# Optimization experiments

Measured on AMD Instinct MI355X. Metric: run time of the kernel, lower is better.

## Reference

```python
import jax, jax.numpy as jnp
import numpy as np
import math

NUM_HEADS = 20
HEAD_SIZE = 20  # newssize = 400
NEG_INF = -1e9


def setup_inputs() -> dict:
    key = jax.random.key(0)
    ks = jax.random.split(key, 10)
    B, S, L, V, D, M = 512, 100, 30, 50000, 400, 128
    user_click = jax.random.randint(ks[0], (B, S, L), 0, V)
    seq_len = jax.random.randint(ks[1], (B,), 1, S + 1)  # at least 1 valid click
    sc = 1.0 / math.sqrt(D)
    return {
        "user_click": user_click,
        "seq_len": seq_len,
        "emb_table": jax.random.normal(ks[2], (V, D), jnp.float32) * 0.02,
        "wq": jax.random.normal(ks[3], (D, D), jnp.float32) * sc,
        "wk": jax.random.normal(ks[4], (D, D), jnp.float32) * sc,
        "wv": jax.random.normal(ks[5], (D, D), jnp.float32) * sc,
        "fc1_w": jax.random.normal(ks[6], (D, M), jnp.float32) * sc,
        "fc1_b": jnp.zeros((M,), jnp.float32),
        "fc2_w": jax.random.normal(ks[7], (M, 1), jnp.float32) * (1.0 / math.sqrt(M)),
        "fc2_b": jnp.zeros((1,), jnp.float32),
    }


def reference(user_click, seq_len, emb_table, wq, wk, wv, fc1_w, fc1_b, fc2_w, fc2_b):
    B, S, L = user_click.shape
    D = emb_table.shape[1]
    H, Dh = NUM_HEADS, HEAD_SIZE

    # news encoder: mean-pooled token embeddings -> [B, S, D]
    click = jnp.take(emb_table, user_click.reshape(-1, L), axis=0).mean(axis=1)
    click = click.reshape(B, S, D)

    # mask: valid positions get +1.0 (as in the torch code), invalid -1e9
    valid = jnp.arange(S)[None, :] < seq_len[:, None]  # [B, S]
    mask = jnp.where(valid, 1.0, NEG_INF).astype(click.dtype)

    # multi-head self-attention over history
    q = (click @ wq).reshape(B, S, H, Dh).transpose(0, 2, 1, 3)
    k = (click @ wk).reshape(B, S, H, Dh).transpose(0, 2, 1, 3)
    v = (click @ wv).reshape(B, S, H, Dh).transpose(0, 2, 1, 3)
    logits = jnp.einsum("bhqd,bhkd->bhqk", q, k) / math.sqrt(Dh)
    logits = logits + mask[:, None, None, :]
    attn = jax.nn.softmax(logits, axis=-1)
    ctx = jnp.einsum("bhqk,bhkd->bhqd", attn, v)
    ctx = ctx.transpose(0, 2, 1, 3).reshape(B, S, D)  # [B, S, D]

    # additive attention pooling over history positions
    e = jnp.tanh(ctx @ fc1_w + fc1_b)            # [B, S, M]
    alpha = e @ fc2_w + fc2_b + mask[:, :, None]  # [B, S, 1]
    w = jax.nn.softmax(alpha, axis=1)
    return jnp.sum(w * ctx, axis=1)               # [B, D]
```

## Files before the change

### kernel.cpp

```cpp
#include <hip/hip_runtime.h>
#include <hip/hip_bf16.h>

using u16 = unsigned short;
using u32 = unsigned int;

#define BB 512
#define SS 100
#define LL 30
#define DD 400
#define MM 128
#define HH 20
#define DHH 20

typedef short v8s __attribute__((ext_vector_type(8)));
typedef float v4f __attribute__((ext_vector_type(4)));

__device__ __forceinline__ float lo2f(u32 u) { return __uint_as_float(u << 16); }
__device__ __forceinline__ float hi2f(u32 u) { return __uint_as_float(u & 0xffff0000u); }
__device__ __forceinline__ float bf2f(u16 h) { return __uint_as_float(((u32)h) << 16); }
__device__ __forceinline__ u16 f2bf(float f) {
  u32 u = __float_as_uint(f);
  u += 0x7fffu + ((u >> 16) & 1u);
  return (u16)(u >> 16);
}
__device__ __forceinline__ u32 packf2(float a, float b) {
  return (u32)f2bf(a) | (((u32)f2bf(b)) << 16);
}

__global__ __launch_bounds__(256) void k_slice(const float* __restrict__ emb,
                                               u32* __restrict__ embS) {
  const int tid = blockIdx.x * 256 + threadIdx.x;
  if (tid >= 10000000) return;
  const int c = tid % 25;
  const int row = (tid / 25) % 50000;
  const int slice = tid / (25 * 50000);
  const float2 v = *(const float2*)&emb[(size_t)row * DD + (slice * 25 + c) * 2];
  embS[tid] = packf2(v.x, v.y);
}

__global__ __launch_bounds__(256) void k_warm(const uint4* __restrict__ embS4,
                                              float* __restrict__ alpha,
                                              float* __restrict__ sink) {
  const int slice = blockIdx.x & 7;
  const int blk = blockIdx.x >> 3;
  const int gid = blockIdx.x * 256 + threadIdx.x;
  const int gstride = gridDim.x * 256;
  for (int i = gid; i < 51200; i += gstride) alpha[i] = 0.f;
  u32 s = 0;
  const int base = slice * 312500;
  for (int i = blk * 256 + threadIdx.x; i < 312500; i += 320 * 256) {
    const uint4 v = embS4[base + i];
    s += v.x ^ v.y ^ v.z ^ v.w;
  }
  if (s == 0x12345678u) sink[0] = 1.f;
}

__global__ __launch_bounds__(256) void k_trans_all(const float* __restrict__ wq,
    const float* __restrict__ wk, const float* __restrict__ wv,
    const float* __restrict__ f1w, u16* __restrict__ wt, u16* __restrict__ wtf) {
  __shared__ float ts[32][33];
  const int z = blockIdx.z;
  const float* src = (z == 0) ? wq : (z == 1) ? wk : (z == 2) ? wv : f1w;
  u16* dst = (z < 3) ? (wt + (size_t)z * 160000) : wtf;
  const int N = (z < 3) ? 400 : 128;
  const int K = 400;
  const int t = threadIdx.x;
  const int n0 = blockIdx.x * 32, k0 = blockIdx.y * 32;
  const int c = t & 31, r8 = t >> 5;
#pragma unroll
  for (int i = 0; i < 4; ++i) {
    const int k = k0 + r8 + i * 8, n = n0 + c;
    ts[r8 + i * 8][c] = (k < K && n < N) ? src[(size_t)k * N + n] : 0.f;
  }
  __syncthreads();
#pragma unroll
  for (int i = 0; i < 4; ++i) {
    const int n = n0 + r8 + i * 8, k = k0 + c;
    if (n < N && k < K) dst[(size_t)n * K + k] = f2bf(ts[c][r8 + i * 8]);
  }
}

__global__ __launch_bounds__(256) void k_embed_s(const int* __restrict__ uc,
                                                 const u32* __restrict__ embS,
                                                 u32* __restrict__ click) {
  __shared__ int sIdx[600];
  const int slice = blockIdx.x & 7;
  const int chunk = blockIdx.x >> 3;
  const int bs0 = chunk * 20;
  const int t = threadIdx.x;
  for (int i = t; i < 600; i += 256) sIdx[i] = uc[(size_t)bs0 * LL + i];
  __syncthreads();
  if (t >= 250) return;
  const int g = t / 25, c = t % 25;
  const u32* base = embS + (size_t)slice * 50000u * 25u + c;
  float a0 = 0.f, a1 = 0.f, b0 = 0.f, b1 = 0.f;
  const int* i0 = &sIdx[g * 30];
  const int* i1 = &sIdx[(g + 10) * 30];
#pragma unroll 6
  for (int l = 0; l < LL; ++l) {
    const u32 v0 = base[(size_t)i0[l] * 25];
    const u32 v1 = base[(size_t)i1[l] * 25];
    a0 += lo2f(v0); a1 += hi2f(v0);
    b0 += lo2f(v1); b1 += hi2f(v1);
  }
  const float s = 1.0f / (float)LL;
  click[(size_t)(bs0 + g) * 200 + slice * 25 + c]      = packf2(a0 * s, a1 * s);
  click[(size_t)(bs0 + g + 10) * 200 + slice * 25 + c] = packf2(b0 * s, b1 * s);
}

__global__ __launch_bounds__(256) void k_qkv_mfma(const u16* __restrict__ A,
    const u16* __restrict__ Wt, u16* __restrict__ C) {
  __shared__ u16 As[256][40];
  __shared__ u16 Bs[80][40];
  const int t = threadIdx.x;
  const int wave = t >> 6, lane = t & 63;
  const int q = lane >> 4, l16 = lane & 15;
  const int m0 = blockIdx.x * 256;
  const int mat = blockIdx.y / 5, ntile = blockIdx.y % 5;
  const int nb = ntile * 80;
  const u16* Bt = Wt + (size_t)(mat * 400 + nb) * 400;
  const int mw = wave * 64;

  v4f acc[4][5];
#pragma unroll
  for (int i = 0; i < 4; ++i)
#pragma unroll
    for (int j = 0; j < 5; ++j) acc[i][j] = (v4f){0.f, 0.f, 0.f, 0.f};

  for (int kt = 0; kt < 13; ++kt) {
    const int k0 = kt * 32;
#pragma unroll
    for (int i = 0; i < 4; ++i) {
      const int id = i * 256 + t;
      const int r = id >> 2, ko = (id & 3) * 8;
      uint4 val = make_uint4(0u, 0u, 0u, 0u);
      if (k0 + ko < 400) val = *(const uint4*)&A[(size_t)(m0 + r) * 400 + k0 + ko];
      *(uint4*)&As[r][ko] = val;
    }
#pragma unroll
    for (int i = 0; i < 2; ++i) {
      const int id = i * 256 + t;
      if (id < 320) {
        const int n = id >> 2, ko = (id & 3) * 8;
        uint4 val = make_uint4(0u, 0u, 0u, 0u);
        if (k0 + ko < 400) val = *(const uint4*)&Bt[(size_t)n * 400 + k0 + ko];
        *(uint4*)&Bs[n][ko] = val;
      }
    }
    __syncthreads();
    v8s a[4], b[5];
#pragma unroll
    for (int ms = 0; ms < 4; ++ms) a[ms] = *(const v8s*)&As[mw + ms * 16 + l16][q * 8];
#pragma unroll
    for (int ns = 0; ns < 5; ++ns) b[ns] = *(const v8s*)&Bs[ns * 16 + l16][q * 8];
#pragma unroll
    for (int ms = 0; ms < 4; ++ms)
#pragma unroll
      for (int ns = 0; ns < 5; ++ns)
        acc[ms][ns] = __builtin_amdgcn_mfma_f32_16x16x32_bf16(a[ms], b[ns], acc[ms][ns], 0, 0, 0);
    __syncthreads();
  }
#pragma unroll
  for (int ms = 0; ms < 4; ++ms)
#pragma unroll
    for (int ns = 0; ns < 5; ++ns) {
      const v4f c = acc[ms][ns];
      const int gcol = mat * 400 + nb + ns * 16 + l16;
#pragma unroll
      for (int reg = 0; reg < 4; ++reg) {
        const int m = m0 + mw + ms * 16 + q * 4 + reg;
        C[(size_t)m * 1200 + gcol] = f2bf(c[reg]);
      }
    }
}

__global__ __launch_bounds__(256) void k_vt(const u32* __restrict__ c32,
                                            u32* __restrict__ vout) {
  __shared__ u16 Vs[4][100][22];
  const int wave = threadIdx.x >> 6, lane = threadIdx.x & 63;
  const int c = blockIdx.x * 4 + wave;
  const int h = c >> 9, b = c & 511;
  const u32* in = c32 + (size_t)b * 60000 + 400 + h * 10;
  u32* out = vout + (size_t)c * 1000;
  for (int i = lane; i < 1000; i += 64) {
    const int s = i / 10, dp = i % 10;
    *(u32*)&Vs[wave][s][dp * 2] = in[s * 600 + dp];
  }
  __syncthreads();
  for (int o = lane; o < 1000; o += 64) {
    const int d = o / 50, sc = o % 50;
    out[o] = (u32)Vs[wave][2 * sc][d] | (((u32)Vs[wave][2 * sc + 1][d]) << 16);
  }
}

__global__ __launch_bounds__(256) void k_attn_mfma(const u32* __restrict__ c32,
    const u16* __restrict__ vtg, const int* __restrict__ seq,
    u16* __restrict__ ctxg) {
  __shared__ u32 Ks[2240];
  const int b = blockIdx.x / HH, h = blockIdx.x % HH;
  const int t = threadIdx.x;
  const int wave = t >> 6, lane = t & 63;
  const int quad = lane >> 4, l16 = lane & 15;
  const int len = seq[b];
  const u32* qp = c32 + (size_t)b * 60000 + h * 10;
  const u32* kp = qp + 200;
  const u32* vb = (const u32*)(vtg + (size_t)(h * 512 + b) * 2000);

  uint2 vfr[2][7];
#pragma unroll
  for (int dt = 0; dt < 2; ++dt) {
    const int d = dt * 16 + l16;
#pragma unroll
    for (int nt = 0; nt < 7; ++nt)
      vfr[dt][nt] = *(const uint2*)(vb + d * 50 + nt * 8 + quad * 2);
  }
  for (int id = t; id < 2240; id += 256) {
    const int r = id / 20, c = id % 20;
    Ks[id] = (r < 100 && c < 10) ? kp[(size_t)r * 600 + c] : 0u;
  }
  __syncthreads();

  const float sc = 0.2236067977499790f;
  u16* cb = ctxg + (size_t)b * SS * DD + h * DHH;
  for (int mi = 0; mi < 2; ++mi) {
    const int mt = wave + mi * 4;
    if (mt >= 7) break;
    const int qrow = mt * 16 + l16;
    const int qr = (qrow < 100) ? qrow : 0;
    union { uint2 u[2]; v8s v; } qf;
    qf.u[0] = *(const uint2*)(qp + (size_t)qr * 600 + quad * 4);
    qf.u[1] = *(const uint2*)(qp + (size_t)qr * 600 + quad * 4 + 2);
    v4f acc[7];
#pragma unroll
    for (int nt = 0; nt < 7; ++nt) {
      const v8s kf = *(const v8s*)&Ks[(nt * 16 + l16) * 20 + quad * 4];
      acc[nt] = __builtin_amdgcn_mfma_f32_16x16x32_bf16(kf, qf.v, (v4f){0.f,0.f,0.f,0.f}, 0, 0, 0);
    }
    float mx = -3.0e38f;
#pragma unroll
    for (int nt = 0; nt < 7; ++nt)
#pragma unroll
      for (int reg = 0; reg < 4; ++reg) {
        const int k = nt * 16 + quad * 4 + reg;
        const float v = acc[nt][reg] * sc + ((k < len) ? 1.0f : -1e9f);
        acc[nt][reg] = v;
        mx = fmaxf(mx, v);
      }
    mx = fmaxf(mx, __shfl_xor(mx, 16));
    mx = fmaxf(mx, __shfl_xor(mx, 32));
    float sum = 0.f;
#pragma unroll
    for (int nt = 0; nt < 7; ++nt)
#pragma unroll
      for (int reg = 0; reg < 4; ++reg) {
        const float e = __expf(acc[nt][reg] - mx);
        acc[nt][reg] = e;
        sum += e;
      }
    sum += __shfl_xor(sum, 16);
    sum += __shfl_xor(sum, 32);
    const float inv = 1.0f / sum;
    v4f o0 = (v4f){0.f, 0.f, 0.f, 0.f}, o1 = o0;
#pragma unroll
    for (int nt = 0; nt < 7; ++nt) {
      union { u32 u[4]; v8s v; } pa, vb0, vb1;
      pa.u[0] = packf2(acc[nt][0] * inv, acc[nt][1] * inv);
      pa.u[1] = packf2(acc[nt][2] * inv, acc[nt][3] * inv);
      pa.u[2] = 0u; pa.u[3] = 0u;
      vb0.u[0] = vfr[0][nt].x; vb0.u[1] = vfr[0][nt].y; vb0.u[2] = 0u; vb0.u[3] = 0u;
      vb1.u[0] = vfr[1][nt].x; vb1.u[1] = vfr[1][nt].y; vb1.u[2] = 0u; vb1.u[3] = 0u;
      o0 = __builtin_amdgcn_mfma_f32_16x16x32_bf16(pa.v, vb0.v, o0, 0, 0, 0);
      o1 = __builtin_amdgcn_mfma_f32_16x16x32_bf16(pa.v, vb1.v, o1, 0, 0, 0);
    }
#pragma unroll
    for (int reg = 0; reg < 4; ++reg) {
      const int q = mt * 16 + quad * 4 + reg;
      if (q < 100) {
        cb[(size_t)q * DD + l16] = f2bf(o0[reg]);
        if (l16 < 4) cb[(size_t)q * DD + 16 + l16] = f2bf(o1[reg]);
      }
    }
  }
}

__global__ __launch_bounds__(256) void k_fc1_alpha(const u16* __restrict__ A,
    const u16* __restrict__ Bt, const float* __restrict__ f1b,
    const float* __restrict__ f2w, float* __restrict__ alpha) {
  __shared__ u16 As[128][40];
  __shared__ u16 Bs[64][40];
  const int t = threadIdx.x;
  const int wave = t >> 6, lane = t & 63;
  const int quad = lane >> 4, l16 = lane & 15;
  const int m0 = blockIdx.x * 128;
  const int nb = blockIdx.y * 64;
  const int mw = wave * 32;
  v4f acc[2][4];
#pragma unroll
  for (int i = 0; i < 2; ++i)
#pragma unroll
    for (int j = 0; j < 4; ++j) acc[i][j] = (v4f){0.f, 0.f, 0.f, 0.f};

  for (int kt = 0; kt < 13; ++kt) {
    const int k0 = kt * 32;
#pragma unroll
    for (int i = 0; i < 2; ++i) {
      const int id = i * 256 + t;
      const int r = id >> 2, ko = (id & 3) * 8;
      uint4 val = make_uint4(0u, 0u, 0u, 0u);
      if (k0 + ko < 400) val = *(const uint4*)&A[(size_t)(m0 + r) * 400 + k0 + ko];
      *(uint4*)&As[r][ko] = val;
    }
    {
      const int r = t >> 2, ko = (t & 3) * 8;
      uint4 val = make_uint4(0u, 0u, 0u, 0u);
      if (k0 + ko < 400) val = *(const uint4*)&Bt[(size_t)(nb + r) * 400 + k0 + ko];
      *(uint4*)&Bs[r][ko] = val;
    }
    __syncthreads();
    v8s a[2], b[4];
#pragma unroll
    for (int ms = 0; ms < 2; ++ms) a[ms] = *(const v8s*)&As[mw + ms * 16 + l16][quad * 8];
#pragma unroll
    for (int ns = 0; ns < 4; ++ns) b[ns] = *(const v8s*)&Bs[ns * 16 + l16][quad * 8];
#pragma unroll
    for (int ms = 0; ms < 2; ++ms)
#pragma unroll
      for (int ns = 0; ns < 4; ++ns)
        acc[ms][ns] = __builtin_amdgcn_mfma_f32_16x16x32_bf16(a[ms], b[ns], acc[ms][ns], 0, 0, 0);
    __syncthreads();
  }
  float fwv[4], fbv[4];
#pragma unroll
  for (int ns = 0; ns < 4; ++ns) {
    fwv[ns] = f2w[nb + ns * 16 + l16];
    fbv[ns] = f1b[nb + ns * 16 + l16];
  }
#pragma unroll
  for (int ms = 0; ms < 2; ++ms)
#pragma unroll
    for (int reg = 0; reg < 4; ++reg) {
      float p = 0.f;
#pragma unroll
      for (int ns = 0; ns < 4; ++ns)
        p += tanhf(acc[ms][ns][reg] + fbv[ns]) * fwv[ns];
#pragma unroll
      for (int o = 1; o < 16; o <<= 1) p += __shfl_xor(p, o);
      if (l16 == 0)
        atomicAdd(&alpha[m0 + mw + ms * 16 + quad * 4 + reg], p);
    }
}

__global__ __launch_bounds__(256) void k_pool(const float* __restrict__ alpha,
    const float* __restrict__ f2b, const int* __restrict__ seq,
    const u16* __restrict__ ctxg, float* __restrict__ out) {
  const int b = blockIdx.x;
  const int t = threadIdx.x, w = t >> 6, lane = t & 63;
  __shared__ float wts[SS];
  const int len = seq[b];
  const float bias = f2b[0];
  if (t < SS) wts[t] = alpha[b * SS + t] + bias + ((t < len) ? 1.0f : -1e9f);
  __syncthreads();
  if (w == 0) {
    const float v0 = wts[lane];
    const float v1 = (lane + 64 < SS) ? wts[lane + 64] : -3.0e38f;
    float mx = fmaxf(v0, v1);
#pragma unroll
    for (int o = 32; o > 0; o >>= 1) mx = fmaxf(mx, __shfl_xor(mx, o));
    const float e0 = __expf(v0 - mx);
    const float e1 = (lane + 64 < SS) ? __expf(v1 - mx) : 0.f;
    float sm = e0 + e1;
#pragma unroll
    for (int o = 32; o > 0; o >>= 1) sm += __shfl_xor(sm, o);
    const float inv = 1.0f / sm;
    wts[lane] = e0 * inv;
    if (lane + 64 < SS) wts[lane + 64] = e1 * inv;
  }
  __syncthreads();
  for (int d = t; d < DD; d += 256) {
    float acc = 0.f;
    const u16* cb = ctxg + (size_t)b * SS * DD + d;
    for (int s = 0; s < SS; ++s) acc += wts[s] * bf2f(cb[(size_t)s * DD]);
    out[(size_t)b * DD + d] = acc;
  }
}

extern "C" void kernel_launch(void* const* d_in, const int* in_sizes, int n_in,
                              void* d_out, int out_size, void* d_ws, size_t ws_size,
                              hipStream_t stream) {
  const int*   uc  = (const int*)d_in[0];
  const int*   seq = (const int*)d_in[1];
  const float* emb = (const float*)d_in[2];
  const float* wq  = (const float*)d_in[3];
  const float* wk  = (const float*)d_in[4];
  const float* wv  = (const float*)d_in[5];
  const float* f1w = (const float*)d_in[6];
  const float* f1b = (const float*)d_in[7];
  const float* f2w = (const float*)d_in[8];
  const float* f2b = (const float*)d_in[9];
  float* out = (float*)d_out;

  u16* vt      = (u16*)d_ws;
  u32* embS    = (u32*)d_ws;
  u16* wt      = (u16*)d_ws + 20000000ull;
  u16* wtf     = (u16*)d_ws + 20480000ull;
  u16* click16 = wtf + 51200ull;
  u16* c16     = click16 + 20480000ull;
  float* alpha = (float*)(c16 + 61440000ull);
  float* sink  = alpha + 51200ull;

  k_slice<<<39063, 256, 0, stream>>>(emb, embS);
  k_trans_all<<<dim3(13, 13, 4), 256, 0, stream>>>(wq, wk, wv, f1w, wt, wtf);
  k_warm<<<2560, 256, 0, stream>>>((const uint4*)embS, alpha, sink);
  k_embed_s<<<20480, 256, 0, stream>>>(uc, embS, (u32*)click16);
  k_qkv_mfma<<<dim3(200, 15), 256, 0, stream>>>(click16, wt, c16);
  k_vt<<<2560, 256, 0, stream>>>((const u32*)c16, (u32*)vt);
  k_attn_mfma<<<BB * HH, 256, 0, stream>>>((const u32*)c16, vt, seq, click16);
  k_fc1_alpha<<<dim3(400, 2), 256, 0, stream>>>(click16, wtf, f1b, f2w, alpha);
  k_pool<<<BB, 256, 0, stream>>>(alpha, f2b, seq, click16, out);
}
```

Measured before the change: 607.8 us.

## Split embedding gather by row half, swizzle QKV LDS, remap QKV blocks to XCDs

The embedding gather now makes two passes, first over indices in the upper half of the vocabulary and then the lower half. The cache warm kernel now prefetches only the upper half of each slice, so the first pass should hit in cache before the second pass fetches the rest. The QKV GEMM replaces padded LDS tiles with XOR-swizzled 64-wide rows to avoid bank conflicts. It also uses a 1D grid that maps contiguous M tiles onto the same XCD so the A tiles are reused within that XCD's L2. The two-pass gather adds branches and rereads the index list, and the swizzle makes the LDS tiles larger.

Measured after the change: 808.0 us. 32.9% more time.

```diff
diff --git a/kernel.cpp b/kernel.cpp
--- a/kernel.cpp
+++ b/kernel.cpp
@@ -48,7 +48,7 @@
   for (int i = gid; i < 51200; i += gstride) alpha[i] = 0.f;
   u32 s = 0;
   const int base = slice * 312500;
-  for (int i = blk * 256 + threadIdx.x; i < 312500; i += 320 * 256) {
+  for (int i = blk * 256 + threadIdx.x + 156250; i < 312500; i += 320 * 256) {
     const uint4 v = embS4[base + i];
     s += v.x ^ v.y ^ v.z ^ v.w;
   }
@@ -96,12 +96,22 @@
   float a0 = 0.f, a1 = 0.f, b0 = 0.f, b1 = 0.f;
   const int* i0 = &sIdx[g * 30];
   const int* i1 = &sIdx[(g + 10) * 30];
+#pragma unroll
+  for (int pass = 0; pass < 2; ++pass) {
+    const int lo = pass ? 0 : 25000;
+    const int hi = pass ? 25000 : 50000;
 #pragma unroll 6
-  for (int l = 0; l < LL; ++l) {
-    const u32 v0 = base[(size_t)i0[l] * 25];
-    const u32 v1 = base[(size_t)i1[l] * 25];
-    a0 += lo2f(v0); a1 += hi2f(v0);
-    b0 += lo2f(v1); b1 += hi2f(v1);
+    for (int l = 0; l < LL; ++l) {
+      const int r0 = i0[l], r1 = i1[l];
+      if (r0 >= lo && r0 < hi) {
+        const u32 v0 = base[(size_t)r0 * 25];
+        a0 += lo2f(v0); a1 += hi2f(v0);
+      }
+      if (r1 >= lo && r1 < hi) {
+        const u32 v1 = base[(size_t)r1 * 25];
+        b0 += lo2f(v1); b1 += hi2f(v1);
+      }
+    }
   }
   const float s = 1.0f / (float)LL;
   click[(size_t)(bs0 + g) * 200 + slice * 25 + c]      = packf2(a0 * s, a1 * s);
@@ -110,13 +120,16 @@
 
 __global__ __launch_bounds__(256) void k_qkv_mfma(const u16* __restrict__ A,
     const u16* __restrict__ Wt, u16* __restrict__ C) {
-  __shared__ u16 As[256][40];
-  __shared__ u16 Bs[80][40];
+  __shared__ u16 As[256 * 64];
+  __shared__ u16 Bs[80 * 64];
   const int t = threadIdx.x;
   const int wave = t >> 6, lane = t & 63;
   const int q = lane >> 4, l16 = lane & 15;
-  const int m0 = blockIdx.x * 256;
-  const int mat = blockIdx.y / 5, ntile = blockIdx.y % 5;
+  const int bid = blockIdx.x;
+  const int xcd = bid & 7, j = bid >> 3;
+  const int m_local = j / 15, mtn = j % 15;
+  const int m0 = (xcd * 25 + m_local) * 256;
+  const int mat = mtn / 5, ntile = mtn % 5;
   const int nb = ntile * 80;
   const u16* Bt = Wt + (size_t)(mat * 400 + nb) * 400;
   const int mw = wave * 64;
@@ -125,34 +138,40 @@
 #pragma unroll
   for (int i = 0; i < 4; ++i)
 #pragma unroll
-    for (int j = 0; j < 5; ++j) acc[i][j] = (v4f){0.f, 0.f, 0.f, 0.f};
+    for (int j2 = 0; j2 < 5; ++j2) acc[i][j2] = (v4f){0.f, 0.f, 0.f, 0.f};
 
   for (int kt = 0; kt < 13; ++kt) {
     const int k0 = kt * 32;
 #pragma unroll
     for (int i = 0; i < 4; ++i) {
       const int id = i * 256 + t;
-      const int r = id >> 2, ko = (id & 3) * 8;
+      const int r = id >> 2, u = id & 3;
       uint4 val = make_uint4(0u, 0u, 0u, 0u);
-      if (k0 + ko < 400) val = *(const uint4*)&A[(size_t)(m0 + r) * 400 + k0 + ko];
-      *(uint4*)&As[r][ko] = val;
+      if (k0 + u * 8 < 400) val = *(const uint4*)&A[(size_t)(m0 + r) * 400 + k0 + u * 8];
+      *(uint4*)&As[r * 64 + ((u ^ (r & 7)) << 3)] = val;
     }
 #pragma unroll
     for (int i = 0; i < 2; ++i) {
       const int id = i * 256 + t;
       if (id < 320) {
-        const int n = id >> 2, ko = (id & 3) * 8;
+        const int n = id >> 2, u = id & 3;
         uint4 val = make_uint4(0u, 0u, 0u, 0u);
-        if (k0 + ko < 400) val = *(const uint4*)&Bt[(size_t)n * 400 + k0 + ko];
-        *(uint4*)&Bs[n][ko] = val;
+        if (k0 + u * 8 < 400) val = *(const uint4*)&Bt[(size_t)n * 400 + k0 + u * 8];
+        *(uint4*)&Bs[n * 64 + ((u ^ (n & 7)) << 3)] = val;
       }
     }
     __syncthreads();
     v8s a[4], b[5];
 #pragma unroll
-    for (int ms = 0; ms < 4; ++ms) a[ms] = *(const v8s*)&As[mw + ms * 16 + l16][q * 8];
-#pragma unroll
-    for (int ns = 0; ns < 5; ++ns) b[ns] = *(const v8s*)&Bs[ns * 16 + l16][q * 8];
+    for (int ms = 0; ms < 4; ++ms) {
+      const int ra = mw + ms * 16 + l16;
+      a[ms] = *(const v8s*)&As[ra * 64 + ((q ^ (ra & 7)) << 3)];
+    }
+#pragma unroll
+    for (int ns = 0; ns < 5; ++ns) {
+      const int rb = ns * 16 + l16;
+      b[ns] = *(const v8s*)&Bs[rb * 64 + ((q ^ (rb & 7)) << 3)];
+    }
 #pragma unroll
     for (int ms = 0; ms < 4; ++ms)
 #pragma unroll
@@ -274,10 +293,10 @@
     }
 #pragma unroll
     for (int reg = 0; reg < 4; ++reg) {
-      const int q = mt * 16 + quad * 4 + reg;
-      if (q < 100) {
-        cb[(size_t)q * DD + l16] = f2bf(o0[reg]);
-        if (l16 < 4) cb[(size_t)q * DD + 16 + l16] = f2bf(o1[reg]);
+      const int q2 = mt * 16 + quad * 4 + reg;
+      if (q2 < 100) {
+        cb[(size_t)q2 * DD + l16] = f2bf(o0[reg]);
+        if (l16 < 4) cb[(size_t)q2 * DD + 16 + l16] = f2bf(o1[reg]);
       }
     }
   }
@@ -412,7 +431,7 @@
   k_trans_all<<<dim3(13, 13, 4), 256, 0, stream>>>(wq, wk, wv, f1w, wt, wtf);
   k_warm<<<2560, 256, 0, stream>>>((const uint4*)embS, alpha, sink);
   k_embed_s<<<20480, 256, 0, stream>>>(uc, embS, (u32*)click16);
-  k_qkv_mfma<<<dim3(200, 15), 256, 0, stream>>>(click16, wt, c16);
+  k_qkv_mfma<<<3000, 256, 0, stream>>>(click16, wt, c16);
   k_vt<<<2560, 256, 0, stream>>>((const u32*)c16, (u32*)vt);
   k_attn_mfma<<<BB * HH, 256, 0, stream>>>((const u32*)c16, vt, seq, click16);
   k_fc1_alpha<<<dim3(400, 2), 256, 0, stream>>>(click16, wtf, f1b, f2w, alpha);
```
